# Kernel tuning notes

Measured on AMD Instinct MI355X. Metric: run time of the kernel, lower is better.

The kernel has to match this reference:

```python
import jax, jax.numpy as jnp
import numpy as np

B, T, C = 8, 512, 512
H, HKV, D = 8, 4, 64
S_MAX = 128
BASE_FREQ = 10000.0
INIT_SIGMA = 256.0
EPS = 1e-6


def _init_positional_kernel(n_heads, head_dim, s_max, base_freq):
    table_size = 2 * s_max + 1
    deltas = jnp.arange(table_size) - s_max
    d_half = head_dim // 2
    freqs = 1.0 / base_freq ** (jnp.arange(d_half, dtype=jnp.float32) / d_half)
    phases = deltas[:, None].astype(jnp.float32) * freqs[None, :]
    P_single = jnp.concatenate([jnp.cos(phases), jnp.sin(phases)], axis=-1)
    return jnp.tile(P_single[None, :, :], (n_heads, 1, 1))


def setup_inputs() -> dict:
    key = jax.random.key(0)
    ks = jax.random.split(key, 6)
    scale = 0.02
    x = jax.random.normal(ks[0], (B, T, C), dtype=jnp.float32)
    Wq = jax.random.normal(ks[1], (C, H * D), dtype=jnp.float32) * scale
    Wk = jax.random.normal(ks[2], (C, HKV * D), dtype=jnp.float32) * scale
    Wv = jax.random.normal(ks[3], (C, HKV * D), dtype=jnp.float32) * scale
    Wproj = jax.random.normal(ks[4], (C, C), dtype=jnp.float32) * scale
    P = _init_positional_kernel(H, D, S_MAX, BASE_FREQ)
    sigma = jnp.full((H,), INIT_SIGMA, dtype=jnp.float32)
    return {"x": x, "Wq": Wq, "Wk": Wk, "Wv": Wv, "Wproj": Wproj, "P": P, "sigma": sigma}


def _norm(t):
    # nGPT-style: unit norm * sqrt(dim)
    dim = t.shape[-1]
    return t * (jnp.sqrt(float(dim)) * jax.lax.rsqrt((t * t).sum(axis=-1, keepdims=True) + EPS))


def _warped_kernel(P, sigma, T_):
    # P: [H, 2*S_MAX+1, D], sigma: [H] -> P_interp: [H, T, T, D]
    positions = jnp.arange(T_)
    delta = positions[:, None] - positions[None, :]  # [T, T]
    s = jnp.abs(sigma) + 1e-6
    delta_warped = S_MAX * jnp.tanh(delta[None, :, :].astype(jnp.float32) / s[:, None, None])
    delta_table = delta_warped + S_MAX  # [H, T, T]
    idx_lo = jnp.floor(delta_table).astype(jnp.int32)
    idx_hi = idx_lo + 1
    frac = delta_table - idx_lo.astype(P.dtype)
    table_max = 2 * S_MAX
    idx_lo = jnp.clip(idx_lo, 0, table_max)
    idx_hi = jnp.clip(idx_hi, 0, table_max)
    head_idx = jnp.arange(H)[:, None, None]
    P_lo = P[head_idx, idx_lo, :]  # [H, T, T, D]
    P_hi = P[head_idx, idx_hi, :]
    return (1 - frac[..., None]) * P_lo + frac[..., None] * P_hi


def reference(x, Wq, Wk, Wv, Wproj, P, sigma):
    q = (x @ Wq).reshape(B, T, H, D)
    k = (x @ Wk).reshape(B, T, HKV, D)
    v = (x @ Wv).reshape(B, T, HKV, D)
    q, k = _norm(q), _norm(k)
    repeats = H // HKV
    k = jnp.repeat(k, repeats, axis=2)
    v = jnp.repeat(v, repeats, axis=2)
    q = q.transpose(0, 2, 1, 3)  # [B, H, T, D]
    k = k.transpose(0, 2, 1, 3)
    v = v.transpose(0, 2, 1, 3)

    sm_scale = 1.0 / jnp.sqrt(float(D))
    P_interp = _warped_kernel(P, sigma, T)  # [H, T, T, D]
    S = jnp.einsum('bhid,hijd,bhjd->bhij', q, P_interp, k) * sm_scale
    causal_mask = jnp.tril(jnp.ones((T, T), dtype=jnp.bool_))
    S = jnp.where(causal_mask[None, None, :, :], S, jnp.finfo(S.dtype).min)
    A = jax.nn.softmax(S, axis=-1)
    y = A @ v  # [B, H, T, D]
    y = y.transpose(0, 2, 1, 3).reshape(B, T, H * D)
    return y @ Wproj
```

## Files before the change

### kernel.cpp

```cpp
#include <hip/hip_runtime.h>
#include <hip/hip_bf16.h>
#include <math.h>

#define Bb 8
#define Tt 512
#define Cc 512
#define Hh 8
#define HKV 4
#define Dd 64

typedef __attribute__((ext_vector_type(8))) short short8;
typedef __attribute__((ext_vector_type(4))) float float4v;
typedef __attribute__((ext_vector_type(2))) __fp16 h2;
typedef __attribute__((ext_vector_type(8))) __fp16 half8;

__device__ __forceinline__ h2 u2h(unsigned u) {
  union { unsigned u; h2 h; } x; x.u = u; return x.h;
}
__device__ __forceinline__ unsigned h2u(h2 h) {
  union { h2 h; unsigned u; } x; x.h = h; return x.u;
}
__device__ __forceinline__ float fdot2(h2 a, h2 b, float c) {
#if __has_builtin(__builtin_amdgcn_fdot2)
  return __builtin_amdgcn_fdot2(a, b, c, false);
#else
  return fmaf((float)a.x, (float)b.x, fmaf((float)a.y, (float)b.y, c));
#endif
}

__device__ __forceinline__ float wave_reduce_sum(float v) {
#pragma unroll
  for (int off = 32; off > 0; off >>= 1) v += __shfl_xor(v, off, 64);
  return v;
}
__device__ __forceinline__ unsigned pack_bf2(float a, float b) {
  __hip_bfloat162 h = __float22bfloat162_rn(make_float2(a, b));
  return *(unsigned*)&h;
}

__global__ __launch_bounds__(256) void prep(
    const float* __restrict__ x, const float* __restrict__ Wq,
    const float* __restrict__ Wk, const float* __restrict__ Wv,
    const float* __restrict__ Wp, const float* __restrict__ P,
    const float* __restrict__ sigma,
    unsigned short* __restrict__ xb, unsigned short* __restrict__ Wtq,
    unsigned short* __restrict__ Wtp, unsigned short* __restrict__ Pwh) {
  const int bid = blockIdx.x;
  const int t = threadIdx.x;
  if (bid < 1024) {
    int i = (bid * 256 + t) * 8;
    float4 f0 = *(const float4*)&x[i];
    float4 f1 = *(const float4*)&x[i + 4];
    unsigned u[4] = {pack_bf2(f0.x, f0.y), pack_bf2(f0.z, f0.w),
                     pack_bf2(f1.x, f1.y), pack_bf2(f1.z, f1.w)};
    *(uint4*)&xb[i] = *(uint4*)u;
  } else if (bid < 1216) {
    __shared__ float Ts[64][65];
    const int bx = bid - 1024;
    const int k0 = (bx & 7) << 6;
    const int n0 = (bx >> 3) << 6;
    const float* src; int ld, nc0; unsigned short* dst; int ndst;
    if (n0 < 512)       { src = Wq; ld = 512; nc0 = n0;        dst = Wtq; ndst = n0; }
    else if (n0 < 768)  { src = Wk; ld = 256; nc0 = n0 - 512;  dst = Wtq; ndst = n0; }
    else if (n0 < 1024) { src = Wv; ld = 256; nc0 = n0 - 768;  dst = Wtq; ndst = n0; }
    else                { src = Wp; ld = 512; nc0 = n0 - 1024; dst = Wtp; ndst = n0 - 1024; }
    const int r = t >> 4, c4 = (t & 15) << 2;
#pragma unroll
    for (int rr = 0; rr < 4; ++rr) {
      int row = (rr << 4) + r;
      float4 f = *(const float4*)&src[(k0 + row) * ld + nc0 + c4];
      Ts[row][c4] = f.x; Ts[row][c4 + 1] = f.y;
      Ts[row][c4 + 2] = f.z; Ts[row][c4 + 3] = f.w;
    }
    __syncthreads();
#pragma unroll
    for (int rr = 0; rr < 4; ++rr) {
      int nr = (rr << 4) + r;
      unsigned u0 = pack_bf2(Ts[c4][nr], Ts[c4 + 1][nr]);
      unsigned u1 = pack_bf2(Ts[c4 + 2][nr], Ts[c4 + 3][nr]);
      *(uint2*)&dst[(ndst + nr) * 512 + k0 + c4] = make_uint2(u0, u1);
    }
  } else {
    int idx = (bid - 1216) * 256 + t;
    int d = idx & 63;
    int rem = idx >> 6;
    int dd = rem % 1023;
    int h = rem / 1023;
    float s = fabsf(sigma[h]) + 1e-6f;
    float delta = (float)(dd - 511);
    float dt = 128.0f * tanhf(delta / s) + 128.0f;
    float lo = floorf(dt);
    int ilo = (int)lo;
    float frac = dt - lo;
    ilo = max(0, min(ilo, 256));
    int ihi = min(ilo + 1, 256);
    const float* Pb = P + h * 257 * 64;
    float val = (1.0f - frac) * Pb[ilo * 64 + d] + frac * Pb[ihi * 64 + d];
    __fp16 hv = (__fp16)val;
    Pwh[idx] = *(unsigned short*)&hv;
  }
}

__global__ __launch_bounds__(256) void qkv_mfma(
    const unsigned short* __restrict__ xb, const unsigned short* __restrict__ Wt,
    unsigned short* __restrict__ qh, unsigned short* __restrict__ kh,
    unsigned short* __restrict__ vT) {
  __shared__ unsigned short As[64][72];
  __shared__ unsigned short Bs[64][72];
  const int m0 = blockIdx.x * 64;
  const int n0 = blockIdx.y * 64;
  const int t = threadIdx.x;
  const int w = t >> 6, lane = t & 63;
  const int srow = t >> 2, sc = (t & 3) << 4;
  float4v acc[4] = {{0,0,0,0},{0,0,0,0},{0,0,0,0},{0,0,0,0}};
  for (int k0 = 0; k0 < 512; k0 += 64) {
    uint4 a0 = *(const uint4*)&xb[(m0 + srow) * 512 + k0 + sc];
    uint4 a1 = *(const uint4*)&xb[(m0 + srow) * 512 + k0 + sc + 8];
    uint4 b0 = *(const uint4*)&Wt[(n0 + srow) * 512 + k0 + sc];
    uint4 b1 = *(const uint4*)&Wt[(n0 + srow) * 512 + k0 + sc + 8];
    __syncthreads();
    *(uint4*)&As[srow][sc] = a0; *(uint4*)&As[srow][sc + 8] = a1;
    *(uint4*)&Bs[srow][sc] = b0; *(uint4*)&Bs[srow][sc + 8] = b1;
    __syncthreads();
    const int ml = (w << 4) + (lane & 15);
    const int kq = (lane >> 4) << 3;
    short8 aF0 = *(short8*)&As[ml][kq];
    short8 aF1 = *(short8*)&As[ml][kq + 32];
#pragma unroll
    for (int nt = 0; nt < 4; ++nt) {
      const int nl = (nt << 4) + (lane & 15);
      short8 bF0 = *(short8*)&Bs[nl][kq];
      short8 bF1 = *(short8*)&Bs[nl][kq + 32];
      acc[nt] = __builtin_amdgcn_mfma_f32_16x16x32_bf16(aF0, bF0, acc[nt], 0, 0, 0);
      acc[nt] = __builtin_amdgcn_mfma_f32_16x16x32_bf16(aF1, bF1, acc[nt], 0, 0, 0);
    }
  }
  const int lane15 = lane & 15;
  const int rowbase = m0 + (w << 4) + ((lane >> 4) << 2);
  if (n0 < 768) {
#pragma unroll
    for (int r = 0; r < 4; ++r) {
      float ss = 0.0f;
#pragma unroll
      for (int nt = 0; nt < 4; ++nt) ss = fmaf(acc[nt][r], acc[nt][r], ss);
#pragma unroll
      for (int off = 1; off < 16; off <<= 1) ss += __shfl_xor(ss, off, 64);
      float sc2 = 8.0f * rsqrtf(ss + 1e-6f);
      const int row = rowbase + r;
      if (n0 < 512) {
        const int h = n0 >> 6;
#pragma unroll
        for (int nt = 0; nt < 4; ++nt) {
          __fp16 hv = (__fp16)(acc[nt][r] * sc2);
          qh[(row * Hh + h) * Dd + (nt << 4) + lane15] = *(unsigned short*)&hv;
        }
      } else {
        const int hkv = (n0 - 512) >> 6;
#pragma unroll
        for (int nt = 0; nt < 4; ++nt) {
          __fp16 hv = (__fp16)(acc[nt][r] * sc2);
          kh[(row * HKV + hkv) * Dd + (nt << 4) + lane15] = *(unsigned short*)&hv;
        }
      }
    }
  } else {
    const int hkv = (n0 - 768) >> 6;
    const int bb = rowbase >> 9;
    const int trow = rowbase & 511;
#pragma unroll
    for (int nt = 0; nt < 4; ++nt) {
      const int d = (nt << 4) + lane15;
      unsigned u0 = h2u(__builtin_amdgcn_cvt_pkrtz(acc[nt][0], acc[nt][1]));
      unsigned u1 = h2u(__builtin_amdgcn_cvt_pkrtz(acc[nt][2], acc[nt][3]));
      *(uint2*)&vT[((bb * HKV + hkv) * 64 + d) * 512 + trow] = make_uint2(u0, u1);
    }
  }
}

__global__ __launch_bounds__(256) void proj_mfma(
    const unsigned short* __restrict__ yb, const unsigned short* __restrict__ Wt,
    float* __restrict__ out) {
  __shared__ unsigned short As[64][72];
  __shared__ unsigned short Bs[64][72];
  const int m0 = blockIdx.x * 64;
  const int n0 = blockIdx.y * 64;
  const int t = threadIdx.x;
  const int w = t >> 6, lane = t & 63;
  const int srow = t >> 2, sc = (t & 3) << 4;
  float4v acc[4] = {{0,0,0,0},{0,0,0,0},{0,0,0,0},{0,0,0,0}};
  for (int k0 = 0; k0 < 512; k0 += 64) {
    uint4 a0 = *(const uint4*)&yb[(m0 + srow) * 512 + k0 + sc];
    uint4 a1 = *(const uint4*)&yb[(m0 + srow) * 512 + k0 + sc + 8];
    uint4 b0 = *(const uint4*)&Wt[(n0 + srow) * 512 + k0 + sc];
    uint4 b1 = *(const uint4*)&Wt[(n0 + srow) * 512 + k0 + sc + 8];
    __syncthreads();
    *(uint4*)&As[srow][sc] = a0; *(uint4*)&As[srow][sc + 8] = a1;
    *(uint4*)&Bs[srow][sc] = b0; *(uint4*)&Bs[srow][sc + 8] = b1;
    __syncthreads();
    const int ml = (w << 4) + (lane & 15);
    const int kq = (lane >> 4) << 3;
    short8 aF0 = *(short8*)&As[ml][kq];
    short8 aF1 = *(short8*)&As[ml][kq + 32];
#pragma unroll
    for (int nt = 0; nt < 4; ++nt) {
      const int nl = (nt << 4) + (lane & 15);
      short8 bF0 = *(short8*)&Bs[nl][kq];
      short8 bF1 = *(short8*)&Bs[nl][kq + 32];
      acc[nt] = __builtin_amdgcn_mfma_f32_16x16x32_bf16(aF0, bF0, acc[nt], 0, 0, 0);
      acc[nt] = __builtin_amdgcn_mfma_f32_16x16x32_bf16(aF1, bF1, acc[nt], 0, 0, 0);
    }
  }
#pragma unroll
  for (int nt = 0; nt < 4; ++nt) {
    int col = n0 + (nt << 4) + (lane & 15);
#pragma unroll
    for (int r = 0; r < 4; ++r) {
      int row = m0 + (w << 4) + ((lane >> 4) << 2) + r;
      out[row * 512 + col] = acc[nt][r];
    }
  }
}

__global__ __launch_bounds__(256) void attn(
    const unsigned short* __restrict__ qh, const unsigned short* __restrict__ kh,
    const unsigned short* __restrict__ vT, const unsigned short* __restrict__ Pwh,
    unsigned short* __restrict__ yb) {
  __shared__ __fp16 PwS[96][72];
  __shared__ __fp16 pS[32][72];
  __shared__ float lS[32];

  const int t = threadIdx.x;
  const int lane = t & 63;
  const int wu = __builtin_amdgcn_readfirstlane(t >> 6);
  const int bh = blockIdx.x;
  const int b = bh >> 3;
  const int h = bh & 7;
  const int hkv = h >> 1;
  const int i0 = 480 - blockIdx.y * 32;

  float l_lane[8];
#pragma unroll
  for (int r = 0; r < 8; ++r) l_lane[r] = 0.0f;
  float4v oacc[2] = {{0, 0, 0, 0}, {0, 0, 0, 0}};

  const int prow = (wu << 3) + 63 - lane;
  const int i_base = i0 + (wu << 3);
  const unsigned short* qbase = &qh[((b * Tt + i_base) * Hh + h) * Dd];

  const int i16 = (wu & 1) << 4;
  const int dt0 = (wu >> 1) << 1;
  const int lm = lane & 15;
  const int kq = (lane >> 4) << 3;
  const unsigned short* vTbase = &vT[((b * HKV + hkv) * 64) * 512];

  for (int jt0 = 0; jt0 <= i0 + 31; jt0 += 64) {
    __syncthreads();
    {
      int jr = t >> 2, dc = (t & 3) << 4;
      const int pb0 = h * 1023 + (i0 - jt0) + 448;
      const unsigned short* pwp = &Pwh[(pb0 + jr) * 64 + dc];
      *(uint4*)&PwS[jr][dc]     = *(const uint4*)&pwp[0];
      *(uint4*)&PwS[jr][dc + 8] = *(const uint4*)&pwp[8];
      int pr2 = 64 + (t >> 3), dc2 = (t & 7) << 3;
      if (pr2 < 95)
        *(uint4*)&PwS[pr2][dc2] = *(const uint4*)&Pwh[(pb0 + pr2) * 64 + dc2];
    }
    uint4 kr[8];
    {
      const uint4* kp = (const uint4*)&kh[((b * Tt + jt0 + lane) * HKV + hkv) * Dd];
#pragma unroll
      for (int c = 0; c < 8; ++c) kr[c] = kp[c];
    }
    __syncthreads();

    const int j = jt0 + lane;
#pragma unroll
    for (int r = 0; r < 8; ++r) {
      const uint4* qp = (const uint4*)&qbase[r * (Hh * Dd)];
      float sr = 0.0f;
#pragma unroll
      for (int ch = 0; ch < 8; ++ch) {
        uint4 qu = qp[ch];
        uint4 pu = *(uint4*)&PwS[prow + r][ch << 3];
        sr = fdot2(u2h(qu.x) * u2h(pu.x), u2h(kr[ch].x), sr);
        sr = fdot2(u2h(qu.y) * u2h(pu.y), u2h(kr[ch].y), sr);
        sr = fdot2(u2h(qu.z) * u2h(pu.z), u2h(kr[ch].z), sr);
        sr = fdot2(u2h(qu.w) * u2h(pu.w), u2h(kr[ch].w), sr);
      }
      float sv = (j <= i_base + r) ? sr * 0.125f : -1e30f;
      float p = __expf(sv - 6.0f);
      l_lane[r] += p;
      pS[(wu << 3) + r][lane] = (__fp16)p;
    }
    __syncthreads();

    half8 a0 = *(half8*)&pS[i16 + lm][kq];
    half8 a1 = *(half8*)&pS[i16 + lm][kq + 32];
#pragma unroll
    for (int dd = 0; dd < 2; ++dd) {
      const unsigned short* vp = vTbase + (((dt0 + dd) << 4) + lm) * 512 + jt0 + kq;
      half8 b0 = *(const half8*)&vp[0];
      half8 b1 = *(const half8*)&vp[32];
      oacc[dd] = __builtin_amdgcn_mfma_f32_16x16x32_f16(a0, b0, oacc[dd], 0, 0, 0);
      oacc[dd] = __builtin_amdgcn_mfma_f32_16x16x32_f16(a1, b1, oacc[dd], 0, 0, 0);
    }
  }

#pragma unroll
  for (int r = 0; r < 8; ++r) {
    float lr = wave_reduce_sum(l_lane[r]);
    if (lane == r) lS[(wu << 3) + r] = lr;
  }
  __syncthreads();

#pragma unroll
  for (int dd = 0; dd < 2; ++dd) {
    const int d = ((dt0 + dd) << 4) + lm;
#pragma unroll
    for (int r = 0; r < 4; ++r) {
      const int irow = i16 + ((lane >> 4) << 2) + r;
      const float val = oacc[dd][r] / lS[irow];
      __hip_bfloat16 hv = __float2bfloat16(val);
      yb[((b * Tt + i0 + irow) * Hh + h) * Dd + d] = *(unsigned short*)&hv;
    }
  }
}

extern "C" void kernel_launch(void* const* d_in, const int* in_sizes, int n_in,
                              void* d_out, int out_size, void* d_ws, size_t ws_size,
                              hipStream_t stream) {
  const float* x     = (const float*)d_in[0];
  const float* Wq    = (const float*)d_in[1];
  const float* Wk    = (const float*)d_in[2];
  const float* Wv    = (const float*)d_in[3];
  const float* Wproj = (const float*)d_in[4];
  const float* P     = (const float*)d_in[5];
  const float* sigma = (const float*)d_in[6];
  float* out = (float*)d_out;

  float* ws = (float*)d_ws;
  unsigned short* qh  = (unsigned short*)ws;
  unsigned short* kh  = (unsigned short*)(ws + 1048576);
  unsigned short* vT  = (unsigned short*)(ws + 1572864);
  unsigned short* Pwh = (unsigned short*)(ws + 2097152);
  unsigned short* xb  = (unsigned short*)(ws + 2359296);
  unsigned short* yb  = xb;
  unsigned short* Wtq = (unsigned short*)(ws + 3407872);
  unsigned short* Wtp = (unsigned short*)(ws + 3670016);

  prep<<<dim3(3262), 256, 0, stream>>>(x, Wq, Wk, Wv, Wproj, P, sigma,
                                       xb, Wtq, Wtp, Pwh);
  qkv_mfma<<<dim3(64, 16), 256, 0, stream>>>(xb, Wtq, qh, kh, vT);
  attn<<<dim3(64, 16), 256, 0, stream>>>(qh, kh, vT, Pwh, yb);
  proj_mfma<<<dim3(64, 8), 256, 0, stream>>>(yb, Wtp, out);
}
```

Before: 137.3 us.

## Double attention block to 512 threads, halving per-wave query rows and output tiles

The attention kernel now launches 8 waves per block instead of 4. Each wave handles 4 query rows instead of 8 and one 16-wide output d-tile instead of two. The shared-memory fill of the positional window is redistributed over 512 threads. This adds parallelism and latency hiding for the scalar fdot2 score loop. In exchange it doubles the K-tile register loads per block (every wave loads the same K rows) and adds barrier cost across more waves.

```diff
diff --git a/kernel.cpp b/kernel.cpp
--- a/kernel.cpp
+++ b/kernel.cpp
@@ -221,7 +221,7 @@
   }
 }
 
-__global__ __launch_bounds__(256) void attn(
+__global__ __launch_bounds__(512, 8) void attn(
     const unsigned short* __restrict__ qh, const unsigned short* __restrict__ kh,
     const unsigned short* __restrict__ vT, const unsigned short* __restrict__ Pwh,
     unsigned short* __restrict__ yb) {
@@ -238,17 +238,17 @@
   const int hkv = h >> 1;
   const int i0 = 480 - blockIdx.y * 32;
 
-  float l_lane[8];
-#pragma unroll
-  for (int r = 0; r < 8; ++r) l_lane[r] = 0.0f;
-  float4v oacc[2] = {{0, 0, 0, 0}, {0, 0, 0, 0}};
-
-  const int prow = (wu << 3) + 63 - lane;
-  const int i_base = i0 + (wu << 3);
+  float l_lane[4];
+#pragma unroll
+  for (int r = 0; r < 4; ++r) l_lane[r] = 0.0f;
+  float4v oacc = {0, 0, 0, 0};
+
+  const int prow = (wu << 2) + 63 - lane;
+  const int i_base = i0 + (wu << 2);
   const unsigned short* qbase = &qh[((b * Tt + i_base) * Hh + h) * Dd];
 
   const int i16 = (wu & 1) << 4;
-  const int dt0 = (wu >> 1) << 1;
+  const int dt0 = wu >> 1;
   const int lm = lane & 15;
   const int kq = (lane >> 4) << 3;
   const unsigned short* vTbase = &vT[((b * HKV + hkv) * 64) * 512];
@@ -256,14 +256,14 @@
   for (int jt0 = 0; jt0 <= i0 + 31; jt0 += 64) {
     __syncthreads();
     {
-      int jr = t >> 2, dc = (t & 3) << 4;
       const int pb0 = h * 1023 + (i0 - jt0) + 448;
-      const unsigned short* pwp = &Pwh[(pb0 + jr) * 64 + dc];
-      *(uint4*)&PwS[jr][dc]     = *(const uint4*)&pwp[0];
-      *(uint4*)&PwS[jr][dc + 8] = *(const uint4*)&pwp[8];
-      int pr2 = 64 + (t >> 3), dc2 = (t & 7) << 3;
-      if (pr2 < 95)
-        *(uint4*)&PwS[pr2][dc2] = *(const uint4*)&Pwh[(pb0 + pr2) * 64 + dc2];
+      int r0 = t >> 3, c0 = (t & 7) << 3;
+      *(uint4*)&PwS[r0][c0] = *(const uint4*)&Pwh[(pb0 + r0) * 64 + c0];
+      int s2 = t + 512;
+      if (s2 < 760) {
+        int r2 = s2 >> 3, c2 = (s2 & 7) << 3;
+        *(uint4*)&PwS[r2][c2] = *(const uint4*)&Pwh[(pb0 + r2) * 64 + c2];
+      }
     }
     uint4 kr[8];
     {
@@ -275,7 +275,7 @@
 
     const int j = jt0 + lane;
 #pragma unroll
-    for (int r = 0; r < 8; ++r) {
+    for (int r = 0; r < 4; ++r) {
       const uint4* qp = (const uint4*)&qbase[r * (Hh * Dd)];
       float sr = 0.0f;
 #pragma unroll
@@ -290,39 +290,33 @@
       float sv = (j <= i_base + r) ? sr * 0.125f : -1e30f;
       float p = __expf(sv - 6.0f);
       l_lane[r] += p;
-      pS[(wu << 3) + r][lane] = (__fp16)p;
+      pS[(wu << 2) + r][lane] = (__fp16)p;
     }
     __syncthreads();
 
     half8 a0 = *(half8*)&pS[i16 + lm][kq];
     half8 a1 = *(half8*)&pS[i16 + lm][kq + 32];
-#pragma unroll
-    for (int dd = 0; dd < 2; ++dd) {
-      const unsigned short* vp = vTbase + (((dt0 + dd) << 4) + lm) * 512 + jt0 + kq;
-      half8 b0 = *(const half8*)&vp[0];
-      half8 b1 = *(const half8*)&vp[32];
-      oacc[dd] = __builtin_amdgcn_mfma_f32_16x16x32_f16(a0, b0, oacc[dd], 0, 0, 0);
-      oacc[dd] = __builtin_amdgcn_mfma_f32_16x16x32_f16(a1, b1, oacc[dd], 0, 0, 0);
-    }
-  }
-
-#pragma unroll
-  for (int r = 0; r < 8; ++r) {
+    const unsigned short* vp = vTbase + ((dt0 << 4) + lm) * 512 + jt0 + kq;
+    half8 b0 = *(const half8*)&vp[0];
+    half8 b1 = *(const half8*)&vp[32];
+    oacc = __builtin_amdgcn_mfma_f32_16x16x32_f16(a0, b0, oacc, 0, 0, 0);
+    oacc = __builtin_amdgcn_mfma_f32_16x16x32_f16(a1, b1, oacc, 0, 0, 0);
+  }
+
+#pragma unroll
+  for (int r = 0; r < 4; ++r) {
     float lr = wave_reduce_sum(l_lane[r]);
-    if (lane == r) lS[(wu << 3) + r] = lr;
+    if (lane == r) lS[(wu << 2) + r] = lr;
   }
   __syncthreads();
 
-#pragma unroll
-  for (int dd = 0; dd < 2; ++dd) {
-    const int d = ((dt0 + dd) << 4) + lm;
-#pragma unroll
-    for (int r = 0; r < 4; ++r) {
-      const int irow = i16 + ((lane >> 4) << 2) + r;
-      const float val = oacc[dd][r] / lS[irow];
-      __hip_bfloat16 hv = __float2bfloat16(val);
-      yb[((b * Tt + i0 + irow) * Hh + h) * Dd + d] = *(unsigned short*)&hv;
-    }
+  const int d = (dt0 << 4) + lm;
+#pragma unroll
+  for (int r = 0; r < 4; ++r) {
+    const int irow = i16 + ((lane >> 4) << 2) + r;
+    const float val = oacc[r] / lS[irow];
+    __hip_bfloat16 hv = __float2bfloat16(val);
+    yb[((b * Tt + i0 + irow) * Hh + h) * Dd + d] = *(unsigned short*)&hv;
   }
 }
 
@@ -351,6 +345,6 @@
   prep<<<dim3(3262), 256, 0, stream>>>(x, Wq, Wk, Wv, Wproj, P, sigma,
                                        xb, Wtq, Wtp, Pwh);
   qkv_mfma<<<dim3(64, 16), 256, 0, stream>>>(xb, Wtq, qh, kh, vT);
-  attn<<<dim3(64, 16), 256, 0, stream>>>(qh, kh, vT, Pwh, yb);
+  attn<<<dim3(64, 16), 512, 0, stream>>>(qh, kh, vT, Pwh, yb);
   proj_mfma<<<dim3(64, 8), 256, 0, stream>>>(yb, Wtp, out);
 }
```

Measured after the change: 155.4 us. 1.13x slower.

## Double-buffer attention tiles and software-pipeline K/Pw loads with deferred PV MFMA

Applied to the files above, without the earlier changes.

The attention loop now double-buffers the positional-kernel and probability tiles in shared memory. It prefetches the next K tile and the next Pw slice into registers while the PV MFMA for the previous tile and the score computation for the current tile run, which cuts the loop from two barriers per iteration to one. Block-row order is also remapped through a permutation constant, so long and short causal rows are interleaved for better load balance. The cost is more LDS and more registers, which could lower occupancy.

```diff
diff --git a/kernel.cpp b/kernel.cpp
--- a/kernel.cpp
+++ b/kernel.cpp
@@ -225,8 +225,8 @@
     const unsigned short* __restrict__ qh, const unsigned short* __restrict__ kh,
     const unsigned short* __restrict__ vT, const unsigned short* __restrict__ Pwh,
     unsigned short* __restrict__ yb) {
-  __shared__ __fp16 PwS[96][72];
-  __shared__ __fp16 pS[32][72];
+  __shared__ __fp16 PwS[2][96][72];
+  __shared__ __fp16 pS[2][32][72];
   __shared__ float lS[32];
 
   const int t = threadIdx.x;
@@ -236,7 +236,8 @@
   const int b = bh >> 3;
   const int h = bh & 7;
   const int hkv = h >> 1;
-  const int i0 = 480 - blockIdx.y * 32;
+  const int i0 = (int)((0x4567BA983210CDEFull >> (blockIdx.y * 4)) & 15) * 32;
+  const int nt = (i0 >> 6) + 1;
 
   float l_lane[8];
 #pragma unroll
@@ -253,25 +254,66 @@
   const int kq = (lane >> 4) << 3;
   const unsigned short* vTbase = &vT[((b * HKV + hkv) * 64) * 512];
 
-  for (int jt0 = 0; jt0 <= i0 + 31; jt0 += 64) {
-    __syncthreads();
-    {
-      int jr = t >> 2, dc = (t & 3) << 4;
-      const int pb0 = h * 1023 + (i0 - jt0) + 448;
-      const unsigned short* pwp = &Pwh[(pb0 + jr) * 64 + dc];
-      *(uint4*)&PwS[jr][dc]     = *(const uint4*)&pwp[0];
-      *(uint4*)&PwS[jr][dc + 8] = *(const uint4*)&pwp[8];
-      int pr2 = 64 + (t >> 3), dc2 = (t & 7) << 3;
-      if (pr2 < 95)
-        *(uint4*)&PwS[pr2][dc2] = *(const uint4*)&Pwh[(pb0 + pr2) * 64 + dc2];
-    }
-    uint4 kr[8];
-    {
-      const uint4* kp = (const uint4*)&kh[((b * Tt + jt0 + lane) * HKV + hkv) * Dd];
-#pragma unroll
-      for (int c = 0; c < 8; ++c) kr[c] = kp[c];
-    }
-    __syncthreads();
+  const int sjr = t >> 2, sdc = (t & 3) << 4;
+  const int spr2 = 64 + (t >> 3), sdc2 = (t & 7) << 3;
+
+  {
+    const int pb0 = h * 1023 + i0 + 448;
+    const unsigned short* pwp = &Pwh[(pb0 + sjr) * 64 + sdc];
+    *(uint4*)&PwS[0][sjr][sdc]     = *(const uint4*)&pwp[0];
+    *(uint4*)&PwS[0][sjr][sdc + 8] = *(const uint4*)&pwp[8];
+    if (spr2 < 95)
+      *(uint4*)&PwS[0][spr2][sdc2] = *(const uint4*)&Pwh[(pb0 + spr2) * 64 + sdc2];
+  }
+  uint4 kr[8];
+  {
+    const uint4* kp = (const uint4*)&kh[((b * Tt + lane) * HKV + hkv) * Dd];
+#pragma unroll
+    for (int c = 0; c < 8; ++c) kr[c] = kp[c];
+  }
+  __syncthreads();
+
+  for (int tt = 0; tt < nt; ++tt) {
+    const int jt0 = tt << 6;
+    const int cb = tt & 1;
+
+    uint4 kr2[8];
+    if (tt + 1 < nt) {
+      const uint4* kp = (const uint4*)&kh[((b * Tt + jt0 + 64 + lane) * HKV + hkv) * Dd];
+#pragma unroll
+      for (int c = 0; c < 8; ++c) kr2[c] = kp[c];
+    }
+    uint4 sw0, sw1, sw2;
+    const bool do_stage = (tt + 1 < nt);
+    if (do_stage) {
+      const int pb0 = h * 1023 + (i0 - jt0 - 64) + 448;
+      const unsigned short* pwp = &Pwh[(pb0 + sjr) * 64 + sdc];
+      sw0 = *(const uint4*)&pwp[0];
+      sw1 = *(const uint4*)&pwp[8];
+      if (spr2 < 95) sw2 = *(const uint4*)&Pwh[(pb0 + spr2) * 64 + sdc2];
+    }
+
+    if (tt > 0) {
+      const int bp = cb ^ 1;
+      const int jp = jt0 - 64;
+      half8 a0 = *(half8*)&pS[bp][i16 + lm][kq];
+      half8 a1 = *(half8*)&pS[bp][i16 + lm][kq + 32];
+#pragma unroll
+      for (int dd = 0; dd < 2; ++dd) {
+        const unsigned short* vp = vTbase + (((dt0 + dd) << 4) + lm) * 512 + jp + kq;
+        half8 b0 = *(const half8*)&vp[0];
+        half8 b1 = *(const half8*)&vp[32];
+        oacc[dd] = __builtin_amdgcn_mfma_f32_16x16x32_f16(a0, b0, oacc[dd], 0, 0, 0);
+        oacc[dd] = __builtin_amdgcn_mfma_f32_16x16x32_f16(a1, b1, oacc[dd], 0, 0, 0);
+      }
+    }
+
+    if (do_stage) {
+      const int sb = cb ^ 1;
+      *(uint4*)&PwS[sb][sjr][sdc]     = sw0;
+      *(uint4*)&PwS[sb][sjr][sdc + 8] = sw1;
+      if (spr2 < 95) *(uint4*)&PwS[sb][spr2][sdc2] = sw2;
+    }
 
     const int j = jt0 + lane;
 #pragma unroll
@@ -281,7 +323,7 @@
 #pragma unroll
       for (int ch = 0; ch < 8; ++ch) {
         uint4 qu = qp[ch];
-        uint4 pu = *(uint4*)&PwS[prow + r][ch << 3];
+        uint4 pu = *(uint4*)&PwS[cb][prow + r][ch << 3];
         sr = fdot2(u2h(qu.x) * u2h(pu.x), u2h(kr[ch].x), sr);
         sr = fdot2(u2h(qu.y) * u2h(pu.y), u2h(kr[ch].y), sr);
         sr = fdot2(u2h(qu.z) * u2h(pu.z), u2h(kr[ch].z), sr);
@@ -290,15 +332,24 @@
       float sv = (j <= i_base + r) ? sr * 0.125f : -1e30f;
       float p = __expf(sv - 6.0f);
       l_lane[r] += p;
-      pS[(wu << 3) + r][lane] = (__fp16)p;
-    }
-    __syncthreads();
-
-    half8 a0 = *(half8*)&pS[i16 + lm][kq];
-    half8 a1 = *(half8*)&pS[i16 + lm][kq + 32];
+      pS[cb][(wu << 3) + r][lane] = (__fp16)p;
+    }
+
+    if (tt + 1 < nt) {
+#pragma unroll
+      for (int c = 0; c < 8; ++c) kr[c] = kr2[c];
+    }
+    __syncthreads();
+  }
+
+  {
+    const int bp = (nt - 1) & 1;
+    const int jp = (nt - 1) << 6;
+    half8 a0 = *(half8*)&pS[bp][i16 + lm][kq];
+    half8 a1 = *(half8*)&pS[bp][i16 + lm][kq + 32];
 #pragma unroll
     for (int dd = 0; dd < 2; ++dd) {
-      const unsigned short* vp = vTbase + (((dt0 + dd) << 4) + lm) * 512 + jt0 + kq;
+      const unsigned short* vp = vTbase + (((dt0 + dd) << 4) + lm) * 512 + jp + kq;
       half8 b0 = *(const half8*)&vp[0];
       half8 b1 = *(const half8*)&vp[32];
       oacc[dd] = __builtin_amdgcn_mfma_f32_16x16x32_f16(a0, b0, oacc[dd], 0, 0, 0);
```

Measured after the change: 139.9 us. Within noise of the previous version (+1.9%).

## Enlarge QKV GEMM tiles to 128x128 and fold softmax scale into q

Applied to the files above, without the earlier changes.

The QKV projection kernel now computes 128x128 output tiles per block, with each wave owning a 64x64 sub-tile of 4x4 MFMA accumulators. This raises operand reuse from shared memory and cuts the number of global tile loads. The 1/sqrt(D) score scale is folded into q when it is written, which removes a multiply per score in the attention inner loop. The trade-offs are fewer blocks (256 instead of 1024), which may underfill the GPU, and higher register pressure from the 16 accumulators.

```diff
diff --git a/kernel.cpp b/kernel.cpp
--- a/kernel.cpp
+++ b/kernel.cpp
@@ -105,74 +105,94 @@
     const unsigned short* __restrict__ xb, const unsigned short* __restrict__ Wt,
     unsigned short* __restrict__ qh, unsigned short* __restrict__ kh,
     unsigned short* __restrict__ vT) {
-  __shared__ unsigned short As[64][72];
-  __shared__ unsigned short Bs[64][72];
-  const int m0 = blockIdx.x * 64;
-  const int n0 = blockIdx.y * 64;
+  __shared__ unsigned short As[128][72];
+  __shared__ unsigned short Bs[128][72];
+  const int m0 = blockIdx.x * 128;
+  const int n0 = blockIdx.y * 128;
   const int t = threadIdx.x;
   const int w = t >> 6, lane = t & 63;
-  const int srow = t >> 2, sc = (t & 3) << 4;
-  float4v acc[4] = {{0,0,0,0},{0,0,0,0},{0,0,0,0},{0,0,0,0}};
+  const int wr = (w >> 1) << 6;
+  const int wc = (w & 1) << 6;
+  const int l15 = lane & 15;
+  const int kq = (lane >> 4) << 3;
+  float4v acc[4][4] = {};
   for (int k0 = 0; k0 < 512; k0 += 64) {
-    uint4 a0 = *(const uint4*)&xb[(m0 + srow) * 512 + k0 + sc];
-    uint4 a1 = *(const uint4*)&xb[(m0 + srow) * 512 + k0 + sc + 8];
-    uint4 b0 = *(const uint4*)&Wt[(n0 + srow) * 512 + k0 + sc];
-    uint4 b1 = *(const uint4*)&Wt[(n0 + srow) * 512 + k0 + sc + 8];
-    __syncthreads();
-    *(uint4*)&As[srow][sc] = a0; *(uint4*)&As[srow][sc + 8] = a1;
-    *(uint4*)&Bs[srow][sc] = b0; *(uint4*)&Bs[srow][sc + 8] = b1;
-    __syncthreads();
-    const int ml = (w << 4) + (lane & 15);
-    const int kq = (lane >> 4) << 3;
-    short8 aF0 = *(short8*)&As[ml][kq];
-    short8 aF1 = *(short8*)&As[ml][kq + 32];
-#pragma unroll
-    for (int nt = 0; nt < 4; ++nt) {
-      const int nl = (nt << 4) + (lane & 15);
-      short8 bF0 = *(short8*)&Bs[nl][kq];
-      short8 bF1 = *(short8*)&Bs[nl][kq + 32];
-      acc[nt] = __builtin_amdgcn_mfma_f32_16x16x32_bf16(aF0, bF0, acc[nt], 0, 0, 0);
-      acc[nt] = __builtin_amdgcn_mfma_f32_16x16x32_bf16(aF1, bF1, acc[nt], 0, 0, 0);
-    }
-  }
-  const int lane15 = lane & 15;
-  const int rowbase = m0 + (w << 4) + ((lane >> 4) << 2);
-  if (n0 < 768) {
-#pragma unroll
-    for (int r = 0; r < 4; ++r) {
-      float ss = 0.0f;
-#pragma unroll
-      for (int nt = 0; nt < 4; ++nt) ss = fmaf(acc[nt][r], acc[nt][r], ss);
-#pragma unroll
-      for (int off = 1; off < 16; off <<= 1) ss += __shfl_xor(ss, off, 64);
-      float sc2 = 8.0f * rsqrtf(ss + 1e-6f);
-      const int row = rowbase + r;
-      if (n0 < 512) {
-        const int h = n0 >> 6;
-#pragma unroll
-        for (int nt = 0; nt < 4; ++nt) {
-          __fp16 hv = (__fp16)(acc[nt][r] * sc2);
-          qh[(row * Hh + h) * Dd + (nt << 4) + lane15] = *(unsigned short*)&hv;
-        }
-      } else {
-        const int hkv = (n0 - 512) >> 6;
-#pragma unroll
-        for (int nt = 0; nt < 4; ++nt) {
-          __fp16 hv = (__fp16)(acc[nt][r] * sc2);
-          kh[(row * HKV + hkv) * Dd + (nt << 4) + lane15] = *(unsigned short*)&hv;
+    uint4 a[4], b[4];
+#pragma unroll
+    for (int i = 0; i < 4; ++i) {
+      int c = (i << 8) + t, r = c >> 3, cc = (c & 7) << 3;
+      a[i] = *(const uint4*)&xb[(m0 + r) * 512 + k0 + cc];
+      b[i] = *(const uint4*)&Wt[(n0 + r) * 512 + k0 + cc];
+    }
+    __syncthreads();
+#pragma unroll
+    for (int i = 0; i < 4; ++i) {
+      int c = (i << 8) + t, r = c >> 3, cc = (c & 7) << 3;
+      *(uint4*)&As[r][cc] = a[i];
+      *(uint4*)&Bs[r][cc] = b[i];
+    }
+    __syncthreads();
+#pragma unroll
+    for (int kk = 0; kk < 2; ++kk) {
+      short8 aF[4];
+#pragma unroll
+      for (int mt = 0; mt < 4; ++mt)
+        aF[mt] = *(short8*)&As[wr + (mt << 4) + l15][kq + (kk << 5)];
+#pragma unroll
+      for (int nt = 0; nt < 4; ++nt) {
+        short8 bF = *(short8*)&Bs[wc + (nt << 4) + l15][kq + (kk << 5)];
+#pragma unroll
+        for (int mt = 0; mt < 4; ++mt)
+          acc[mt][nt] = __builtin_amdgcn_mfma_f32_16x16x32_bf16(aF[mt], bF, acc[mt][nt], 0, 0, 0);
+      }
+    }
+  }
+  const int nc0 = n0 + wc;
+  const int rowq = (lane >> 4) << 2;
+  if (nc0 < 768) {
+#pragma unroll
+    for (int mt = 0; mt < 4; ++mt) {
+#pragma unroll
+      for (int r = 0; r < 4; ++r) {
+        float ss = 0.0f;
+#pragma unroll
+        for (int nt = 0; nt < 4; ++nt) ss = fmaf(acc[mt][nt][r], acc[mt][nt][r], ss);
+#pragma unroll
+        for (int off = 1; off < 16; off <<= 1) ss += __shfl_xor(ss, off, 64);
+        float sc2 = 8.0f * rsqrtf(ss + 1e-6f);
+        const int row = m0 + wr + (mt << 4) + rowq + r;
+        if (nc0 < 512) {
+          const int h = nc0 >> 6;
+          const float sc3 = sc2 * 0.125f;
+#pragma unroll
+          for (int nt = 0; nt < 4; ++nt) {
+            __fp16 hv = (__fp16)(acc[mt][nt][r] * sc3);
+            qh[(row * Hh + h) * Dd + (nt << 4) + l15] = *(unsigned short*)&hv;
+          }
+        } else {
+          const int hkv = (nc0 - 512) >> 6;
+#pragma unroll
+          for (int nt = 0; nt < 4; ++nt) {
+            __fp16 hv = (__fp16)(acc[mt][nt][r] * sc2);
+            kh[(row * HKV + hkv) * Dd + (nt << 4) + l15] = *(unsigned short*)&hv;
+          }
         }
       }
     }
   } else {
-    const int hkv = (n0 - 768) >> 6;
-    const int bb = rowbase >> 9;
-    const int trow = rowbase & 511;
-#pragma unroll
-    for (int nt = 0; nt < 4; ++nt) {
-      const int d = (nt << 4) + lane15;
-      unsigned u0 = h2u(__builtin_amdgcn_cvt_pkrtz(acc[nt][0], acc[nt][1]));
-      unsigned u1 = h2u(__builtin_amdgcn_cvt_pkrtz(acc[nt][2], acc[nt][3]));
-      *(uint2*)&vT[((bb * HKV + hkv) * 64 + d) * 512 + trow] = make_uint2(u0, u1);
+    const int hkv = (nc0 - 768) >> 6;
+#pragma unroll
+    for (int mt = 0; mt < 4; ++mt) {
+      const int rowbase = m0 + wr + (mt << 4) + rowq;
+      const int bb = rowbase >> 9;
+      const int trow = rowbase & 511;
+#pragma unroll
+      for (int nt = 0; nt < 4; ++nt) {
+        const int d = (nt << 4) + l15;
+        unsigned u0 = h2u(__builtin_amdgcn_cvt_pkrtz(acc[mt][nt][0], acc[mt][nt][1]));
+        unsigned u1 = h2u(__builtin_amdgcn_cvt_pkrtz(acc[mt][nt][2], acc[mt][nt][3]));
+        *(uint2*)&vT[((bb * HKV + hkv) * 64 + d) * 512 + trow] = make_uint2(u0, u1);
+      }
     }
   }
 }
@@ -287,7 +307,7 @@
         sr = fdot2(u2h(qu.z) * u2h(pu.z), u2h(kr[ch].z), sr);
         sr = fdot2(u2h(qu.w) * u2h(pu.w), u2h(kr[ch].w), sr);
       }
-      float sv = (j <= i_base + r) ? sr * 0.125f : -1e30f;
+      float sv = (j <= i_base + r) ? sr : -1e30f;
       float p = __expf(sv - 6.0f);
       l_lane[r] += p;
       pS[(wu << 3) + r][lane] = (__fp16)p;
@@ -350,7 +370,7 @@
 
   prep<<<dim3(3262), 256, 0, stream>>>(x, Wq, Wk, Wv, Wproj, P, sigma,
                                        xb, Wtq, Wtp, Pwh);
-  qkv_mfma<<<dim3(64, 16), 256, 0, stream>>>(xb, Wtq, qh, kh, vT);
+  qkv_mfma<<<dim3(32, 8), 256, 0, stream>>>(xb, Wtq, qh, kh, vT);
   attn<<<dim3(64, 16), 256, 0, stream>>>(qh, kh, vT, Pwh, yb);
   proj_mfma<<<dim3(64, 8), 256, 0, stream>>>(yb, Wtp, out);
 }
```

New measurement: 153.4 us. 1.12x slower.
